# Optimization experiments

Hardware: AMD Instinct MI355X
Metric: run time of the kernel (lower is better)

Reference implementation:

```python
import jax, jax.numpy as jnp
import numpy as np

N, E, B = 50000, 500000, 500
NODE_IN, EDGE_IN = 64, 16
NODE_OUT, EDGE_OUT = 96, 64
FP_DIM, FP_EMBED = 2048, 128
HIDDEN = [512, 512]
OUT = 256
BN_EPS = 1e-5


def setup_inputs() -> dict:
    key = jax.random.key(0)
    ks = jax.random.split(key, 16)
    inp = {
        "node_feats": jax.random.normal(ks[0], (N, NODE_IN), jnp.float32),
        "edge_feats": jax.random.normal(ks[1], (E, EDGE_IN), jnp.float32),
        "fp_vector": jax.random.uniform(ks[2], (B, FP_DIM), jnp.float32),
        "src": jax.random.randint(ks[3], (E,), 0, N, dtype=jnp.int32),
        "dst": jax.random.randint(ks[4], (E,), 0, N, dtype=jnp.int32),
        "graph_ids": jnp.sort(jax.random.randint(ks[5], (N,), 0, B, dtype=jnp.int32)),
        # mpnn stand-in: single node projection
        "W_mpnn": jax.random.normal(ks[6], (NODE_IN, NODE_OUT), jnp.float32) / np.sqrt(NODE_IN),
        "b_mpnn": jnp.zeros((NODE_OUT,), jnp.float32),
        # project_edge_feats_module: linear edge projection
        "W_edge": jax.random.normal(ks[7], (EDGE_IN, EDGE_OUT), jnp.float32) / np.sqrt(EDGE_IN),
        "b_edge": jnp.zeros((EDGE_OUT,), jnp.float32),
        # FingerprintEncoder: Linear + BatchNorm1d (eval) + ReLU (+Dropout off)
        "W_fp": jax.random.normal(ks[8], (FP_DIM, FP_EMBED), jnp.float32) / np.sqrt(FP_DIM),
        "b_fp": jnp.zeros((FP_EMBED,), jnp.float32),
        "bn_gamma": jnp.ones((FP_EMBED,), jnp.float32),
        "bn_beta": jnp.zeros((FP_EMBED,), jnp.float32),
        "bn_mean": jnp.zeros((FP_EMBED,), jnp.float32),
        "bn_var": jnp.ones((FP_EMBED,), jnp.float32),
    }
    d_in = NODE_OUT + EDGE_OUT + FP_EMBED  # gnn_readout_dim + fp_embed_dim
    dims = [d_in] + HIDDEN + [OUT]
    for i in range(len(dims) - 1):
        inp[f"W_ffn{i}"] = jax.random.normal(ks[9 + i], (dims[i], dims[i + 1]), jnp.float32) / np.sqrt(dims[i])
        inp[f"b_ffn{i}"] = jnp.zeros((dims[i + 1],), jnp.float32)
    return inp


def reference(node_feats, edge_feats, fp_vector, src, dst, graph_ids,
              W_mpnn, b_mpnn, W_edge, b_edge,
              W_fp, b_fp, bn_gamma, bn_beta, bn_mean, bn_var,
              W_ffn0, b_ffn0, W_ffn1, b_ffn1, W_ffn2, b_ffn2):
    # mpnn node encodings [N, NODE_OUT]
    node_emb = node_feats @ W_mpnn + b_mpnn
    # projected edge embeddings [E, EDGE_OUT]
    edge_emb = edge_feats @ W_edge + b_edge
    # message: gather src node emb, concat edge emb -> [E, NODE_OUT+EDGE_OUT]
    msg = jnp.concatenate([node_emb[src], edge_emb], axis=1)
    # reduce: sum messages per destination node -> [N, NODE_OUT+EDGE_OUT]
    node_msg_sum = jax.ops.segment_sum(msg, dst, num_segments=N)
    # global_sum_pooling over nodes per graph -> [B, NODE_OUT+EDGE_OUT]
    mol = jax.ops.segment_sum(node_msg_sum, graph_ids, num_segments=B)
    mol = jax.nn.softmax(mol, axis=1)
    # fingerprint encoder (eval mode: BN uses running stats, dropout off)
    fp = fp_vector @ W_fp + b_fp
    fp = (fp - bn_mean) * jax.lax.rsqrt(bn_var + BN_EPS) * bn_gamma + bn_beta
    fp = jax.nn.relu(fp)
    # combined FFN (dropout off in eval)
    x = jnp.concatenate([mol, fp], axis=1)
    x = jax.nn.relu(x @ W_ffn0 + b_ffn0)
    x = jax.nn.relu(x @ W_ffn1 + b_ffn1)
    return x @ W_ffn2 + b_ffn2
```

## Files before the change

### kernel.cpp

```cpp
#include <hip/hip_runtime.h>
#include <math.h>

#define NODE_IN 64
#define NODE_OUT 96
#define EDGE_IN 16
#define EDGE_OUT 64
#define ACC_W 80
#define NB 500
#define FPD 2048
#define FPE 128
#define XDIM 288
#define BN_EPS 1e-5f
#define HB 1024
#define NBLKP 512

__global__ __launch_bounds__(1024) void hist_fp_kernel(
    const int* __restrict__ dst, const int* __restrict__ gids,
    int* __restrict__ gkey, int* __restrict__ pbhT, int nblk,
    const float* __restrict__ fpv, const float* __restrict__ Wf,
    const float* __restrict__ bf, const float* __restrict__ gam,
    const float* __restrict__ bet, const float* __restrict__ mu,
    const float* __restrict__ var, float* __restrict__ xbuf, int E)
{
    __shared__ int   h[NB];
    __shared__ float part[7][4][FPE];
    const int t = threadIdx.x;

    if (blockIdx.x >= nblk) {
        const int j  = t & 127;
        const int kh = __builtin_amdgcn_readfirstlane(t >> 7);
        const int r0 = (blockIdx.x - nblk) * 4;
        const int k0 = kh * 256;

        const float* __restrict__ xp0 = fpv + (size_t)(r0 + 0) * FPD + k0;
        const float* __restrict__ xp1 = fpv + (size_t)(r0 + 1) * FPD + k0;
        const float* __restrict__ xp2 = fpv + (size_t)(r0 + 2) * FPD + k0;
        const float* __restrict__ xp3 = fpv + (size_t)(r0 + 3) * FPD + k0;
        const float* __restrict__ wp  = Wf + (size_t)k0 * FPE + j;

        float a0 = 0.f, a1 = 0.f, a2 = 0.f, a3 = 0.f;
        for (int k = 0; k < 256; k += 8) {
            #pragma unroll
            for (int u = 0; u < 8; ++u) {
                const float w = wp[(size_t)(k + u) * FPE];
                a0 = fmaf(xp0[k + u], w, a0);
                a1 = fmaf(xp1[k + u], w, a1);
                a2 = fmaf(xp2[k + u], w, a2);
                a3 = fmaf(xp3[k + u], w, a3);
            }
        }
        if (kh > 0) {
            part[kh - 1][0][j] = a0; part[kh - 1][1][j] = a1;
            part[kh - 1][2][j] = a2; part[kh - 1][3][j] = a3;
        }
        __syncthreads();
        if (kh == 0) {
            #pragma unroll
            for (int qd = 0; qd < 7; ++qd) {
                a0 += part[qd][0][j]; a1 += part[qd][1][j];
                a2 += part[qd][2][j]; a3 += part[qd][3][j];
            }
            const float sc = rsqrtf(var[j] + BN_EPS) * gam[j];
            const float sh = bet[j] - mu[j] * sc;
            const float bj = bf[j];
            xbuf[(size_t)(r0 + 0) * XDIM + 160 + j] = fmaxf(fmaf(a0 + bj, sc, sh), 0.f);
            xbuf[(size_t)(r0 + 1) * XDIM + 160 + j] = fmaxf(fmaf(a1 + bj, sc, sh), 0.f);
            xbuf[(size_t)(r0 + 2) * XDIM + 160 + j] = fmaxf(fmaf(a2 + bj, sc, sh), 0.f);
            xbuf[(size_t)(r0 + 3) * XDIM + 160 + j] = fmaxf(fmaf(a3 + bj, sc, sh), 0.f);
        }
        return;
    }

    for (int i = t; i < NB; i += 1024) h[i] = 0;
    __syncthreads();
    const int e = blockIdx.x * HB + t;
    if (e < E) {
        const int g = gids[dst[e]];
        gkey[e] = g;
        atomicAdd(&h[g], 1);
    }
    __syncthreads();
    for (int i = t; i < NB; i += 1024)
        pbhT[(size_t)i * NBLKP + blockIdx.x] = h[i];
}

__global__ __launch_bounds__(512) void colscan_kernel(
    const int* __restrict__ pbhT, int* __restrict__ pcs,
    int* __restrict__ gsum, int nblk)
{
    __shared__ int s[512];
    const int g = blockIdx.x;
    const int t = threadIdx.x;
    const int v0 = (t < nblk) ? pbhT[(size_t)g * NBLKP + t] : 0;
    s[t] = v0;
    __syncthreads();
    for (int d = 1; d < 512; d <<= 1) {
        const int v = (t >= d) ? s[t - d] : 0;
        __syncthreads();
        s[t] += v;
        __syncthreads();
    }
    if (t < nblk) pcs[(size_t)t * NB + g] = s[t] - v0;
    if (t == 511) gsum[g] = s[511];
}

__global__ __launch_bounds__(1024) void scatter2_kernel(
    const int* __restrict__ gkey, const int* __restrict__ src,
    const int* __restrict__ pcs, const int* __restrict__ gsum,
    int2* __restrict__ sp, int* __restrict__ offs, int E)
{
    __shared__ int sc[512];
    __shared__ int offsL[NB];
    __shared__ int h[NB];
    __shared__ int basel[NB];
    const int t = threadIdx.x;

    int v0 = 0;
    if (t < 512) {
        v0 = (t < NB) ? gsum[t] : 0;
        sc[t] = v0;
    }
    __syncthreads();
    for (int d = 1; d < 512; d <<= 1) {
        int v = 0;
        if (t < 512 && t >= d) v = sc[t - d];
        __syncthreads();
        if (t < 512) sc[t] += v;
        __syncthreads();
    }
    if (t < NB) offsL[t] = sc[t] - v0;
    __syncthreads();

    for (int i = t; i < NB; i += 1024) {
        h[i] = 0;
        basel[i] = offsL[i] + pcs[(size_t)blockIdx.x * NB + i];
    }
    if (blockIdx.x == 0 && t < NB) offs[t] = offsL[t];
    __syncthreads();

    const int e = blockIdx.x * HB + t;
    if (e < E) {
        const int g = gkey[e];
        const int r = atomicAdd(&h[g], 1);
        sp[basel[g] + r] = make_int2(src[e], e);
    }
}

__global__ __launch_bounds__(1024) void graph_accum(
    const int2* __restrict__ sp,
    const float* __restrict__ nf, const float* __restrict__ ef,
    const int* __restrict__ offs, const int* __restrict__ tot,
    const float* __restrict__ Wm, const float* __restrict__ bm,
    const float* __restrict__ We, const float* __restrict__ be,
    float* __restrict__ xbuf, int E)
{
    const int g = blockIdx.x;
    const int t = threadIdx.x;
    const int lane = t & 63;
    const int w = t >> 6;
    const int start = offs[g];
    const int cnt = tot[g];
    const int end = start + cnt;

    const float4* __restrict__ nf4 = (const float4*)nf;
    const float4* __restrict__ ef4 = (const float4*)ef;

    __shared__ float sacc[16][ACC_W];
    __shared__ float accRow[ACC_W];
    __shared__ float red[1024];

    const int eidx  = lane >> 4;
    const int chunk = lane & 15;
    const int eidx2 = lane >> 2;
    const int comp  = lane & 3;

    float nacc0 = 0.f, nacc1 = 0.f, nacc2 = 0.f, nacc3 = 0.f;
    float eacc0 = 0.f, eacc1 = 0.f, eacc2 = 0.f, eacc3 = 0.f;

    for (int p0 = start + w * 64; p0 < end; p0 += 1024) {
        const int lim = min(64, end - p0);
        const int2 pr = sp[min(p0 + lane, E - 1)];
        const int sv = pr.x, ev = pr.y;

        #pragma unroll
        for (int r = 0; r < 4; ++r) {
            float4 v[4];
            int ee[4];
            #pragma unroll
            for (int u = 0; u < 4; ++u) {
                ee[u] = (r * 4 + u) * 4 + eidx;
                const int s = __shfl(sv, ee[u]);
                v[u] = nf4[(size_t)s * 16 + chunk];
            }
            #pragma unroll
            for (int u = 0; u < 4; ++u) {
                if (ee[u] < lim) {
                    nacc0 += v[u].x; nacc1 += v[u].y;
                    nacc2 += v[u].z; nacc3 += v[u].w;
                }
            }
        }

        {
            float4 v[4];
            int ee[4];
            #pragma unroll
            for (int u = 0; u < 4; ++u) {
                ee[u] = u * 16 + eidx2;
                const int eid = __shfl(ev, ee[u]);
                v[u] = ef4[(size_t)eid * 4 + comp];
            }
            #pragma unroll
            for (int u = 0; u < 4; ++u) {
                if (ee[u] < lim) {
                    eacc0 += v[u].x; eacc1 += v[u].y;
                    eacc2 += v[u].z; eacc3 += v[u].w;
                }
            }
        }
    }

    #pragma unroll
    for (int bit = 16; bit <= 32; bit <<= 1) {
        nacc0 += __shfl_xor(nacc0, bit);
        nacc1 += __shfl_xor(nacc1, bit);
        nacc2 += __shfl_xor(nacc2, bit);
        nacc3 += __shfl_xor(nacc3, bit);
    }
    #pragma unroll
    for (int bit = 4; bit <= 32; bit <<= 1) {
        eacc0 += __shfl_xor(eacc0, bit);
        eacc1 += __shfl_xor(eacc1, bit);
        eacc2 += __shfl_xor(eacc2, bit);
        eacc3 += __shfl_xor(eacc3, bit);
    }
    if (lane < 16) {
        sacc[w][lane * 4 + 0] = nacc0;
        sacc[w][lane * 4 + 1] = nacc1;
        sacc[w][lane * 4 + 2] = nacc2;
        sacc[w][lane * 4 + 3] = nacc3;
    }
    if (lane < 4) {
        sacc[w][NODE_IN + lane * 4 + 0] = eacc0;
        sacc[w][NODE_IN + lane * 4 + 1] = eacc1;
        sacc[w][NODE_IN + lane * 4 + 2] = eacc2;
        sacc[w][NODE_IN + lane * 4 + 3] = eacc3;
    }
    __syncthreads();
    if (t < ACC_W) {
        float s = 0.f;
        #pragma unroll
        for (int w2 = 0; w2 < 16; ++w2) s += sacc[w2][t];
        accRow[t] = s;
    }
    __syncthreads();

    const float cntf = (float)cnt;
    float mr = 0.f;
    if (t < 96) {
        float m2 = 0.f;
        for (int k = 0; k < NODE_IN; ++k) m2 = fmaf(accRow[k], Wm[k * NODE_OUT + t], m2);
        mr = m2 + cntf * bm[t];
    } else if (t < 160) {
        const int j = t - 96;
        float m2 = 0.f;
        for (int k = 0; k < EDGE_IN; ++k) m2 = fmaf(accRow[NODE_IN + k], We[k * EDGE_OUT + j], m2);
        mr = m2 + cntf * be[j];
    }

    red[t] = (t < 160) ? mr : -1e30f;
    __syncthreads();
    for (int st = 512; st > 0; st >>= 1) {
        if (t < st) red[t] = fmaxf(red[t], red[t + st]);
        __syncthreads();
    }
    const float mx = red[0];
    __syncthreads();
    const float evx = (t < 160) ? expf(mr - mx) : 0.f;
    red[t] = evx;
    __syncthreads();
    for (int st = 512; st > 0; st >>= 1) {
        if (t < st) red[t] += red[t + st];
        __syncthreads();
    }
    if (t < 160) xbuf[(size_t)g * XDIM + t] = evx / red[0];
}

template<int NO, int KS>
__global__ __launch_bounds__(1024) void ffn_split(
    const float* __restrict__ X, const float* __restrict__ W,
    const float* __restrict__ bias, float* __restrict__ Y,
    int Bv, int Ni, int doRelu)
{
    __shared__ float part[KS - 1][4][NO];
    const int t = threadIdx.x;
    const int col = t % NO;
    const int ks = __builtin_amdgcn_readfirstlane(t / NO);
    const int r0 = blockIdx.x * 4;
    const int kchunk = Ni / KS;
    const int k0 = ks * kchunk;

    const float* __restrict__ xp0 = X + (size_t)(r0 + 0) * Ni + k0;
    const float* __restrict__ xp1 = X + (size_t)(r0 + 1) * Ni + k0;
    const float* __restrict__ xp2 = X + (size_t)(r0 + 2) * Ni + k0;
    const float* __restrict__ xp3 = X + (size_t)(r0 + 3) * Ni + k0;
    const float* __restrict__ wp  = W + (size_t)k0 * NO + col;

    float a0 = 0.f, a1 = 0.f, a2 = 0.f, a3 = 0.f;
    for (int k = 0; k < kchunk; k += 8) {
        #pragma unroll
        for (int u = 0; u < 8; ++u) {
            const float w = wp[(size_t)(k + u) * NO];
            a0 = fmaf(xp0[k + u], w, a0);
            a1 = fmaf(xp1[k + u], w, a1);
            a2 = fmaf(xp2[k + u], w, a2);
            a3 = fmaf(xp3[k + u], w, a3);
        }
    }
    if (ks > 0) {
        part[ks - 1][0][col] = a0; part[ks - 1][1][col] = a1;
        part[ks - 1][2][col] = a2; part[ks - 1][3][col] = a3;
    }
    __syncthreads();
    if (ks == 0) {
        #pragma unroll
        for (int qd = 0; qd < KS - 1; ++qd) {
            a0 += part[qd][0][col]; a1 += part[qd][1][col];
            a2 += part[qd][2][col]; a3 += part[qd][3][col];
        }
        const float bv = bias[col];
        float o0 = a0 + bv, o1 = a1 + bv, o2 = a2 + bv, o3 = a3 + bv;
        if (doRelu) {
            o0 = fmaxf(o0, 0.f); o1 = fmaxf(o1, 0.f);
            o2 = fmaxf(o2, 0.f); o3 = fmaxf(o3, 0.f);
        }
        Y[(size_t)(r0 + 0) * NO + col] = o0;
        if (r0 + 1 < Bv) Y[(size_t)(r0 + 1) * NO + col] = o1;
        if (r0 + 2 < Bv) Y[(size_t)(r0 + 2) * NO + col] = o2;
        if (r0 + 3 < Bv) Y[(size_t)(r0 + 3) * NO + col] = o3;
    }
}

extern "C" void kernel_launch(void* const* d_in, const int* in_sizes, int n_in,
                              void* d_out, int out_size, void* d_ws, size_t ws_size,
                              hipStream_t stream)
{
    const float* node_feats = (const float*)d_in[0];
    const float* edge_feats = (const float*)d_in[1];
    const float* fpv        = (const float*)d_in[2];
    const int*   src        = (const int*)d_in[3];
    const int*   dst        = (const int*)d_in[4];
    const int*   gids       = (const int*)d_in[5];
    const float* Wm  = (const float*)d_in[6];
    const float* bm  = (const float*)d_in[7];
    const float* We  = (const float*)d_in[8];
    const float* be  = (const float*)d_in[9];
    const float* Wf  = (const float*)d_in[10];
    const float* bf  = (const float*)d_in[11];
    const float* gam = (const float*)d_in[12];
    const float* bet = (const float*)d_in[13];
    const float* mu  = (const float*)d_in[14];
    const float* var = (const float*)d_in[15];
    const float* W0  = (const float*)d_in[16];
    const float* b0  = (const float*)d_in[17];
    const float* W1  = (const float*)d_in[18];
    const float* b1  = (const float*)d_in[19];
    const float* W2  = (const float*)d_in[20];
    const float* b2  = (const float*)d_in[21];
    const int E = in_sizes[3];
    const int nblk = (E + HB - 1) / HB;

    float* xbuf  = (float*)d_ws;
    int2*  sp    = (int2*)(xbuf + (size_t)NB * XDIM);
    int*   gkey  = (int*)(sp + E);
    int*   pbhT  = gkey + E;
    int*   pcs   = pbhT + (size_t)NB * NBLKP;
    int*   gsum  = pcs + (size_t)nblk * NB;
    int*   offs  = gsum + NB;
    float* h1    = (float*)(offs + NB);
    float* h2    = h1 + (size_t)NB * 512;

    hipLaunchKernelGGL(hist_fp_kernel, dim3(nblk + NB / 4), dim3(1024), 0, stream,
                       dst, gids, gkey, pbhT, nblk,
                       fpv, Wf, bf, gam, bet, mu, var, xbuf, E);
    hipLaunchKernelGGL(colscan_kernel, dim3(NB), dim3(512), 0, stream,
                       pbhT, pcs, gsum, nblk);
    hipLaunchKernelGGL(scatter2_kernel, dim3(nblk), dim3(1024), 0, stream,
                       gkey, src, pcs, gsum, sp, offs, E);
    hipLaunchKernelGGL(graph_accum, dim3(NB), dim3(1024), 0, stream,
                       sp, node_feats, edge_feats, offs, gsum,
                       Wm, bm, We, be, xbuf, E);
    hipLaunchKernelGGL((ffn_split<512, 2>), dim3((NB + 3) / 4), dim3(1024), 0, stream,
                       xbuf, W0, b0, h1, NB, XDIM, 1);
    hipLaunchKernelGGL((ffn_split<512, 2>), dim3((NB + 3) / 4), dim3(1024), 0, stream,
                       h1, W1, b1, h2, NB, 512, 1);
    hipLaunchKernelGGL((ffn_split<256, 4>), dim3((NB + 3) / 4), dim3(1024), 0, stream,
                       h2, W2, b2, (float*)d_out, NB, 512, 0);
}
```

Baseline: 112.5 us.

## Split FP encoder and FFN GEMMs across more blocks with column tiling

The fingerprint GEMM is split over four K-slices across four times as many blocks. Each slice writes partial sums to a workspace buffer, and the colscan kernel adds the slices and applies bias, BatchNorm and ReLU. The FFN layers move from one block per four rows over all columns to a 2D grid of 128-column tiles with an eight-way K split, so the grid gets more blocks and uses more CUs. The cost is extra partial-sum traffic and more redundant reads of X per column tile. The row-bound checks are dropped, which relies on NB being a multiple of four.

```diff
diff --git a/kernel.cpp b/kernel.cpp
--- a/kernel.cpp
+++ b/kernel.cpp
@@ -18,19 +18,20 @@
     const int* __restrict__ dst, const int* __restrict__ gids,
     int* __restrict__ gkey, int* __restrict__ pbhT, int nblk,
     const float* __restrict__ fpv, const float* __restrict__ Wf,
-    const float* __restrict__ bf, const float* __restrict__ gam,
-    const float* __restrict__ bet, const float* __restrict__ mu,
-    const float* __restrict__ var, float* __restrict__ xbuf, int E)
+    float* __restrict__ pfp, int E)
 {
     __shared__ int   h[NB];
     __shared__ float part[7][4][FPE];
     const int t = threadIdx.x;
 
     if (blockIdx.x >= nblk) {
-        const int j  = t & 127;
-        const int kh = __builtin_amdgcn_readfirstlane(t >> 7);
-        const int r0 = (blockIdx.x - nblk) * 4;
-        const int k0 = kh * 256;
+        const int f   = blockIdx.x - nblk;
+        const int rg  = f >> 2;
+        const int ksl = f & 3;
+        const int r0  = rg * 4;
+        const int j   = t & 127;
+        const int ks  = __builtin_amdgcn_readfirstlane(t >> 7);
+        const int k0  = ksl * 512 + ks * 64;
 
         const float* __restrict__ xp0 = fpv + (size_t)(r0 + 0) * FPD + k0;
         const float* __restrict__ xp1 = fpv + (size_t)(r0 + 1) * FPD + k0;
@@ -39,7 +40,7 @@
         const float* __restrict__ wp  = Wf + (size_t)k0 * FPE + j;
 
         float a0 = 0.f, a1 = 0.f, a2 = 0.f, a3 = 0.f;
-        for (int k = 0; k < 256; k += 8) {
+        for (int k = 0; k < 64; k += 8) {
             #pragma unroll
             for (int u = 0; u < 8; ++u) {
                 const float w = wp[(size_t)(k + u) * FPE];
@@ -49,24 +50,20 @@
                 a3 = fmaf(xp3[k + u], w, a3);
             }
         }
-        if (kh > 0) {
-            part[kh - 1][0][j] = a0; part[kh - 1][1][j] = a1;
-            part[kh - 1][2][j] = a2; part[kh - 1][3][j] = a3;
-        }
-        __syncthreads();
-        if (kh == 0) {
+        if (ks > 0) {
+            part[ks - 1][0][j] = a0; part[ks - 1][1][j] = a1;
+            part[ks - 1][2][j] = a2; part[ks - 1][3][j] = a3;
+        }
+        __syncthreads();
+        if (ks == 0) {
             #pragma unroll
             for (int qd = 0; qd < 7; ++qd) {
                 a0 += part[qd][0][j]; a1 += part[qd][1][j];
                 a2 += part[qd][2][j]; a3 += part[qd][3][j];
             }
-            const float sc = rsqrtf(var[j] + BN_EPS) * gam[j];
-            const float sh = bet[j] - mu[j] * sc;
-            const float bj = bf[j];
-            xbuf[(size_t)(r0 + 0) * XDIM + 160 + j] = fmaxf(fmaf(a0 + bj, sc, sh), 0.f);
-            xbuf[(size_t)(r0 + 1) * XDIM + 160 + j] = fmaxf(fmaf(a1 + bj, sc, sh), 0.f);
-            xbuf[(size_t)(r0 + 2) * XDIM + 160 + j] = fmaxf(fmaf(a2 + bj, sc, sh), 0.f);
-            xbuf[(size_t)(r0 + 3) * XDIM + 160 + j] = fmaxf(fmaf(a3 + bj, sc, sh), 0.f);
+            float* __restrict__ pp = pfp + ((size_t)ksl * NB + r0) * FPE + j;
+            pp[0 * FPE] = a0; pp[1 * FPE] = a1;
+            pp[2 * FPE] = a2; pp[3 * FPE] = a3;
         }
         return;
     }
@@ -86,7 +83,11 @@
 
 __global__ __launch_bounds__(512) void colscan_kernel(
     const int* __restrict__ pbhT, int* __restrict__ pcs,
-    int* __restrict__ gsum, int nblk)
+    int* __restrict__ gsum, int nblk,
+    const float* __restrict__ pfp, const float* __restrict__ bf,
+    const float* __restrict__ gam, const float* __restrict__ bet,
+    const float* __restrict__ mu, const float* __restrict__ var,
+    float* __restrict__ xbuf)
 {
     __shared__ int s[512];
     const int g = blockIdx.x;
@@ -102,6 +103,16 @@
     }
     if (t < nblk) pcs[(size_t)t * NB + g] = s[t] - v0;
     if (t == 511) gsum[g] = s[511];
+
+    if (t < FPE) {
+        const float a = (pfp[((size_t)0 * NB + g) * FPE + t] +
+                         pfp[((size_t)1 * NB + g) * FPE + t]) +
+                        (pfp[((size_t)2 * NB + g) * FPE + t] +
+                         pfp[((size_t)3 * NB + g) * FPE + t]);
+        const float sc = rsqrtf(var[t] + BN_EPS) * gam[t];
+        const float sh = bet[t] - mu[t] * sc;
+        xbuf[(size_t)g * XDIM + 160 + t] = fmaxf(fmaf(a + bf[t], sc, sh), 0.f);
+    }
 }
 
 __global__ __launch_bounds__(1024) void scatter2_kernel(
@@ -286,30 +297,31 @@
     if (t < 160) xbuf[(size_t)g * XDIM + t] = evx / red[0];
 }
 
-template<int NO, int KS>
-__global__ __launch_bounds__(1024) void ffn_split(
+template<int NO>
+__global__ __launch_bounds__(1024) void ffn_tile(
     const float* __restrict__ X, const float* __restrict__ W,
     const float* __restrict__ bias, float* __restrict__ Y,
-    int Bv, int Ni, int doRelu)
-{
-    __shared__ float part[KS - 1][4][NO];
+    int Ni, int doRelu)
+{
+    __shared__ float part[7][4][128];
     const int t = threadIdx.x;
-    const int col = t % NO;
-    const int ks = __builtin_amdgcn_readfirstlane(t / NO);
+    const int col = t & 127;
+    const int ks = __builtin_amdgcn_readfirstlane(t >> 7);
     const int r0 = blockIdx.x * 4;
-    const int kchunk = Ni / KS;
+    const int cg = blockIdx.y * 128 + col;
+    const int kchunk = Ni >> 3;
     const int k0 = ks * kchunk;
 
     const float* __restrict__ xp0 = X + (size_t)(r0 + 0) * Ni + k0;
     const float* __restrict__ xp1 = X + (size_t)(r0 + 1) * Ni + k0;
     const float* __restrict__ xp2 = X + (size_t)(r0 + 2) * Ni + k0;
     const float* __restrict__ xp3 = X + (size_t)(r0 + 3) * Ni + k0;
-    const float* __restrict__ wp  = W + (size_t)k0 * NO + col;
+    const float* __restrict__ wp  = W + (size_t)k0 * NO + cg;
 
     float a0 = 0.f, a1 = 0.f, a2 = 0.f, a3 = 0.f;
-    for (int k = 0; k < kchunk; k += 8) {
+    for (int k = 0; k < kchunk; k += 4) {
         #pragma unroll
-        for (int u = 0; u < 8; ++u) {
+        for (int u = 0; u < 4; ++u) {
             const float w = wp[(size_t)(k + u) * NO];
             a0 = fmaf(xp0[k + u], w, a0);
             a1 = fmaf(xp1[k + u], w, a1);
@@ -324,20 +336,20 @@
     __syncthreads();
     if (ks == 0) {
         #pragma unroll
-        for (int qd = 0; qd < KS - 1; ++qd) {
+        for (int qd = 0; qd < 7; ++qd) {
             a0 += part[qd][0][col]; a1 += part[qd][1][col];
             a2 += part[qd][2][col]; a3 += part[qd][3][col];
         }
-        const float bv = bias[col];
+        const float bv = bias[cg];
         float o0 = a0 + bv, o1 = a1 + bv, o2 = a2 + bv, o3 = a3 + bv;
         if (doRelu) {
             o0 = fmaxf(o0, 0.f); o1 = fmaxf(o1, 0.f);
             o2 = fmaxf(o2, 0.f); o3 = fmaxf(o3, 0.f);
         }
-        Y[(size_t)(r0 + 0) * NO + col] = o0;
-        if (r0 + 1 < Bv) Y[(size_t)(r0 + 1) * NO + col] = o1;
-        if (r0 + 2 < Bv) Y[(size_t)(r0 + 2) * NO + col] = o2;
-        if (r0 + 3 < Bv) Y[(size_t)(r0 + 3) * NO + col] = o3;
+        Y[(size_t)(r0 + 0) * NO + cg] = o0;
+        Y[(size_t)(r0 + 1) * NO + cg] = o1;
+        Y[(size_t)(r0 + 2) * NO + cg] = o2;
+        Y[(size_t)(r0 + 3) * NO + cg] = o3;
     }
 }
 
@@ -377,23 +389,25 @@
     int*   pcs   = pbhT + (size_t)NB * NBLKP;
     int*   gsum  = pcs + (size_t)nblk * NB;
     int*   offs  = gsum + NB;
-    float* h1    = (float*)(offs + NB);
+    float* pfp   = (float*)(offs + NB);
+    float* h1    = pfp + (size_t)4 * NB * FPE;
     float* h2    = h1 + (size_t)NB * 512;
 
-    hipLaunchKernelGGL(hist_fp_kernel, dim3(nblk + NB / 4), dim3(1024), 0, stream,
+    hipLaunchKernelGGL(hist_fp_kernel, dim3(nblk + NB), dim3(1024), 0, stream,
                        dst, gids, gkey, pbhT, nblk,
-                       fpv, Wf, bf, gam, bet, mu, var, xbuf, E);
+                       fpv, Wf, pfp, E);
     hipLaunchKernelGGL(colscan_kernel, dim3(NB), dim3(512), 0, stream,
-                       pbhT, pcs, gsum, nblk);
+                       pbhT, pcs, gsum, nblk,
+                       pfp, bf, gam, bet, mu, var, xbuf);
     hipLaunchKernelGGL(scatter2_kernel, dim3(nblk), dim3(1024), 0, stream,
                        gkey, src, pcs, gsum, sp, offs, E);
     hipLaunchKernelGGL(graph_accum, dim3(NB), dim3(1024), 0, stream,
                        sp, node_feats, edge_feats, offs, gsum,
                        Wm, bm, We, be, xbuf, E);
-    hipLaunchKernelGGL((ffn_split<512, 2>), dim3((NB + 3) / 4), dim3(1024), 0, stream,
-                       xbuf, W0, b0, h1, NB, XDIM, 1);
-    hipLaunchKernelGGL((ffn_split<512, 2>), dim3((NB + 3) / 4), dim3(1024), 0, stream,
-                       h1, W1, b1, h2, NB, 512, 1);
-    hipLaunchKernelGGL((ffn_split<256, 4>), dim3((NB + 3) / 4), dim3(1024), 0, stream,
-                       h2, W2, b2, (float*)d_out, NB, 512, 0);
-}
+    hipLaunchKernelGGL((ffn_tile<512>), dim3(NB / 4, 4), dim3(1024), 0, stream,
+                       xbuf, W0, b0, h1, XDIM, 1);
+    hipLaunchKernelGGL((ffn_tile<512>), dim3(NB / 4, 4), dim3(1024), 0, stream,
+                       h1, W1, b1, h2, 512, 1);
+    hipLaunchKernelGGL((ffn_tile<256>), dim3(NB / 4, 2), dim3(1024), 0, stream,
+                       h2, W2, b2, (float*)d_out, 512, 0);
+}
```

Result: faster. 93.98 us (-16.5%).
